# Performance work log

Hardware: AMD Instinct MI355X
Metric: run time of the kernel (lower is better)

Reference implementation:

```python
import jax, jax.numpy as jnp
import numpy as np

B, H, W, C, WS, SHIFT, NH = 64, 14, 14, 1024, 7, 3, 32
HD = C // NH
SCALE = HD ** -0.5

def _rel_index():
    coords = np.stack(np.meshgrid(np.arange(WS), np.arange(WS), indexing='ij'))  # [2,ws,ws]
    flat = coords.reshape(2, -1)
    rel = (flat[:, :, None] - flat[:, None, :]).transpose(1, 2, 0)  # [49,49,2]
    rel[:, :, 0] += WS - 1
    rel[:, :, 1] += WS - 1
    rel[:, :, 0] *= 2 * WS - 1
    return jnp.asarray(rel.sum(-1))  # [49,49] int

REL_IDX = _rel_index()

def _shift_mask():
    m = np.zeros((H, W), np.float32)
    cnt = 0
    for hs in (slice(0, -WS), slice(-WS, -SHIFT), slice(-SHIFT, None)):
        for ws_ in (slice(0, -WS), slice(-WS, -SHIFT), slice(-SHIFT, None)):
            m[hs, ws_] = cnt
            cnt += 1
    mw = m.reshape(H // WS, WS, W // WS, WS).transpose(0, 2, 1, 3).reshape(-1, WS * WS)
    diff = mw[:, None, :] - mw[:, :, None]
    return jnp.asarray(np.where(diff != 0, -100.0, 0.0).astype(np.float32))  # [nW,49,49]

ATTN_MASK = _shift_mask()

def layernorm(x, g, b, eps=1e-5):
    mu = x.mean(-1, keepdims=True)
    var = ((x - mu) ** 2).mean(-1, keepdims=True)
    return (x - mu) * jax.lax.rsqrt(var + eps) * g + b

def window_partition(x):  # [B,H,W,C] -> [B*nW, 49, C]
    x = x.reshape(B, H // WS, WS, W // WS, WS, C)
    return x.transpose(0, 1, 3, 2, 4, 5).reshape(-1, WS * WS, C)

def window_reverse(x):  # [B*nW, 49, C] -> [B,H,W,C]
    x = x.reshape(B, H // WS, W // WS, WS, WS, C)
    return x.transpose(0, 1, 3, 2, 4, 5).reshape(B, H, W, C)

def swin_block(x, p, shift):
    (ln1_g, ln1_b, qkv_w, qkv_b, rpb, proj_w, proj_b,
     ln2_g, ln2_b, fc1_w, fc1_b, fc2_w, fc2_b) = p
    h = layernorm(x, ln1_g, ln1_b).reshape(B, H, W, C)
    if shift:
        h = jnp.roll(h, (-SHIFT, -SHIFT), axis=(1, 2))
    hw = window_partition(h)                              # [Bn,49,C]
    qkv = hw @ qkv_w + qkv_b                              # [Bn,49,3C]
    q, k, v = qkv.reshape(-1, WS * WS, 3, NH, HD).transpose(2, 0, 3, 1, 4)  # each [Bn,NH,49,HD]
    attn = jnp.einsum('bhqd,bhkd->bhqk', q * SCALE, k)    # [Bn,NH,49,49]
    attn = attn + rpb[REL_IDX].transpose(2, 0, 1)[None]   # fused rel-pos bias
    if shift:
        nW = ATTN_MASK.shape[0]
        attn = attn.reshape(B, nW, NH, WS * WS, WS * WS) + ATTN_MASK[None, :, None]
        attn = attn.reshape(-1, NH, WS * WS, WS * WS)
    attn = jax.nn.softmax(attn, axis=-1)
    o = jnp.einsum('bhqk,bhkd->bhqd', attn, v).transpose(0, 2, 1, 3).reshape(-1, WS * WS, C)
    o = o @ proj_w + proj_b
    o = window_reverse(o)
    if shift:
        o = jnp.roll(o, (SHIFT, SHIFT), axis=(1, 2))
    x = x + o.reshape(B, H * W, C)
    h2 = layernorm(x, ln2_g, ln2_b)
    return x + jax.nn.gelu(h2 @ fc1_w + fc1_b, approximate=False) @ fc2_w + fc2_b

def setup_inputs() -> dict:
    key = jax.random.key(0)
    ks = iter(jax.random.split(key, 64))
    def rnd(shape, s=0.02):
        return jax.random.normal(next(ks), shape, jnp.float32) * s
    inp = {'x': jax.random.normal(next(ks), (B, H * W, C), jnp.float32)}
    for i in range(2):
        inp[f'b{i}_ln1_g'] = jnp.ones((C,), jnp.float32)
        inp[f'b{i}_ln1_b'] = jnp.zeros((C,), jnp.float32)
        inp[f'b{i}_qkv_w'] = rnd((C, 3 * C))
        inp[f'b{i}_qkv_b'] = jnp.zeros((3 * C,), jnp.float32)
        inp[f'b{i}_rpb'] = rnd(((2 * WS - 1) ** 2, NH))
        inp[f'b{i}_proj_w'] = rnd((C, C))
        inp[f'b{i}_proj_b'] = jnp.zeros((C,), jnp.float32)
        inp[f'b{i}_ln2_g'] = jnp.ones((C,), jnp.float32)
        inp[f'b{i}_ln2_b'] = jnp.zeros((C,), jnp.float32)
        inp[f'b{i}_fc1_w'] = rnd((C, 4 * C))
        inp[f'b{i}_fc1_b'] = jnp.zeros((4 * C,), jnp.float32)
        inp[f'b{i}_fc2_w'] = rnd((4 * C, C))
        inp[f'b{i}_fc2_b'] = jnp.zeros((C,), jnp.float32)
    inp['h_ln_g'] = jnp.ones((C,), jnp.float32)
    inp['h_ln_b'] = jnp.zeros((C,), jnp.float32)
    inp['h_w1'] = rnd((C, 512)); inp['h_b1'] = jnp.zeros((512,), jnp.float32)
    inp['h_w2'] = rnd((512, 128)); inp['h_b2'] = jnp.zeros((128,), jnp.float32)
    inp['h_w3'] = rnd((128, 2)); inp['h_b3'] = jnp.zeros((2,), jnp.float32)
    return inp

def reference(x,
              b0_ln1_g, b0_ln1_b, b0_qkv_w, b0_qkv_b, b0_rpb, b0_proj_w, b0_proj_b,
              b0_ln2_g, b0_ln2_b, b0_fc1_w, b0_fc1_b, b0_fc2_w, b0_fc2_b,
              b1_ln1_g, b1_ln1_b, b1_qkv_w, b1_qkv_b, b1_rpb, b1_proj_w, b1_proj_b,
              b1_ln2_g, b1_ln2_b, b1_fc1_w, b1_fc1_b, b1_fc2_w, b1_fc2_b,
              h_ln_g, h_ln_b, h_w1, h_b1, h_w2, h_b2, h_w3, h_b3):
    p0 = (b0_ln1_g, b0_ln1_b, b0_qkv_w, b0_qkv_b, b0_rpb, b0_proj_w, b0_proj_b,
          b0_ln2_g, b0_ln2_b, b0_fc1_w, b0_fc1_b, b0_fc2_w, b0_fc2_b)
    p1 = (b1_ln1_g, b1_ln1_b, b1_qkv_w, b1_qkv_b, b1_rpb, b1_proj_w, b1_proj_b,
          b1_ln2_g, b1_ln2_b, b1_fc1_w, b1_fc1_b, b1_fc2_w, b1_fc2_b)
    x = swin_block(x, p0, shift=False)
    x = swin_block(x, p1, shift=True)
    pooled = x.mean(axis=1)  # global avg pool -> [B, C]
    h = layernorm(pooled, h_ln_g, h_ln_b)
    h = jax.nn.gelu(h @ h_w1 + h_b1, approximate=False)  # dropout is identity (eval)
    h = jax.nn.gelu(h @ h_w2 + h_b2, approximate=False)
    return h @ h_w3 + h_b3  # [B, num_classes]
```

## Files before the change

### kernel.cpp

```cpp
#include <hip/hip_runtime.h>
#include <hip/hip_bf16.h>
#include <hip/hip_fp16.h>
#include <math.h>

#define BB 64
#define CC 1024
#define NH 32
#define NTOK (BB * 14 * 14)
#define SCALE 0.17677669529663687f

typedef __attribute__((ext_vector_type(8))) short short8;
typedef __attribute__((ext_vector_type(8))) unsigned short us8;
typedef __attribute__((ext_vector_type(4))) float f32x4;

__device__ __align__(16) float  g_X  [(size_t)NTOK * CC];
__device__ __align__(16) unsigned short g_Qh[(size_t)NTOK * 3072];
__device__ __align__(16) unsigned short g_B[(size_t)NTOK * CC];
__device__ __align__(16) unsigned short g_C[(size_t)NTOK * 4096];
__device__ __align__(16) unsigned short g_Wq[(size_t)2*3072*1024];
__device__ __align__(16) unsigned short g_Wp[(size_t)2*1024*1024];
__device__ __align__(16) unsigned short g_W1[(size_t)2*4096*1024];
__device__ __align__(16) unsigned short g_W2[(size_t)2*1024*4096];
__device__ __align__(16) float g_H0[64 * CC];
__device__ __align__(16) float g_H1[64 * 512];
__device__ __align__(16) float g_H2[64 * 128];

__device__ __forceinline__ float gelu_f(float x) {
    return 0.5f * x * (1.0f + erff(x * 0.70710678118654752f));
}

__device__ __forceinline__ unsigned short f16_bits(float v) {
    _Float16 hh = (_Float16)v;
    return *(unsigned short*)&hh;
}
__device__ __forceinline__ float f16_val(unsigned short u) {
    _Float16 h;
    __builtin_memcpy(&h, &u, 2);
    return (float)h;
}

__device__ __forceinline__ int win_to_xrow(int r, int shifted) {
    int bn = r / 49, t = r - bn * 49;
    int b = bn >> 2, w = bn & 3;
    int wh = w >> 1, ww_ = w & 1;
    int th = t / 7, tw = t - th * 7;
    int gh = wh * 7 + th, gw = ww_ * 7 + tw;
    if (shifted) { gh = gh + 3; if (gh >= 14) gh -= 14; gw = gw + 3; if (gw >= 14) gw -= 14; }
    return b * 196 + gh * 14 + gw;
}

__device__ __forceinline__ void gload_lds16(const void* g, void* l) {
    __builtin_amdgcn_global_load_lds(
        (const __attribute__((address_space(1))) unsigned int*)g,
        (__attribute__((address_space(3))) unsigned int*)l, 16, 0, 0);
}

__global__ __launch_bounds__(256) void convw_kernel(const float* __restrict__ W,
    unsigned short* __restrict__ Wh, int K, int N)
{
    __shared__ float t[32][33];
    int n0 = blockIdx.x * 32, k0 = blockIdx.y * 32;
    int tx = threadIdx.x & 31, ty = threadIdx.x >> 5;
    #pragma unroll
    for (int i = 0; i < 4; ++i)
        t[ty + 8 * i][tx] = W[(size_t)(k0 + ty + 8 * i) * N + n0 + tx];
    __syncthreads();
    #pragma unroll
    for (int i = 0; i < 4; ++i) {
        int n = ty + 8 * i;
        Wh[(size_t)(n0 + n) * K + k0 + tx] = f16_bits(t[tx][n]);
    }
}

__global__ __launch_bounds__(256) void ln_kernel(const float* __restrict__ X,
    const float* __restrict__ g, const float* __restrict__ bta,
    unsigned short* __restrict__ outh, int shifted, int partition)
{
    int token = blockIdx.x * 4 + (threadIdx.x >> 6);
    int lane = threadIdx.x & 63;
    int xrow = partition ? win_to_xrow(token, shifted) : token;
    const float4* src = (const float4*)(X + (size_t)xrow * CC);
    float4 v[4];
    float s = 0.f;
    #pragma unroll
    for (int w = 0; w < 4; ++w) {
        v[w] = src[w * 64 + lane];
        s += v[w].x + v[w].y + v[w].z + v[w].w;
    }
    #pragma unroll
    for (int o = 32; o; o >>= 1) s += __shfl_xor(s, o);
    float mean = s * (1.0f / CC);
    float ss = 0.f;
    #pragma unroll
    for (int w = 0; w < 4; ++w) {
        float d0 = v[w].x - mean, d1 = v[w].y - mean, d2 = v[w].z - mean, d3 = v[w].w - mean;
        ss += d0 * d0 + d1 * d1 + d2 * d2 + d3 * d3;
    }
    #pragma unroll
    for (int o = 32; o; o >>= 1) ss += __shfl_xor(ss, o);
    float inv = 1.0f / sqrtf(ss * (1.0f / CC) + 1e-5f);
    #pragma unroll
    for (int w = 0; w < 4; ++w) {
        int c4 = w * 64 + lane;
        float4 gv = *(const float4*)(g + c4 * 4);
        float4 bv = *(const float4*)(bta + c4 * 4);
        ushort4 uo;
        uo.x = f16_bits((v[w].x - mean) * inv * gv.x + bv.x);
        uo.y = f16_bits((v[w].y - mean) * inv * gv.y + bv.y);
        uo.z = f16_bits((v[w].z - mean) * inv * gv.z + bv.z);
        uo.w = f16_bits((v[w].w - mean) * inv * gv.w + bv.w);
        *(ushort4*)(outh + (size_t)token * CC + c4 * 4) = uo;
    }
}

template<int EPI>
__global__ __launch_bounds__(256, 2) void gemm_mfma(
    const unsigned short* __restrict__ A, const unsigned short* __restrict__ W,
    const float* __restrict__ bias,
    float* __restrict__ outf, unsigned short* __restrict__ outh,
    int N, int K, int shifted, int NR, int GC)
{
    __shared__ unsigned short sm[EPI <= 1 ? 16896 : 16640];
    const int tid = threadIdx.x;
    const int wave = tid >> 6, lane = tid & 63;
    const int wr = wave >> 1, wc = wave & 1;
    const int nb = gridDim.x;
    const int wg = (blockIdx.x & 7) * (nb >> 3) + (blockIdx.x >> 3);
    const int gsz = GC * NR;
    const int grp = wg / gsz;
    const int rem = wg - grp * gsz;
    const int by = rem / GC;
    const int bx = grp * GC + (rem - by * GC);
    const int row0 = by * 128, col0 = bx * 128;
    const int rsel = lane & 15;

    f32x4 acc[4][4] = {};

    const int srow = tid >> 3, sslot = tid & 7;

    for (int k0 = 0; k0 < K; k0 += 64) {
        #pragma unroll
        for (int i = 0; i < 8; ++i) {
            const int t = i >> 2;
            const int sub = i & 3;
            const int row = sub * 32 + srow;
            const int c = sslot ^ (row & 7);
            const unsigned short* gp = (t == 0) ? A : W;
            const int rb = (t == 0) ? row0 : col0;
            gload_lds16(gp + (size_t)(rb + row) * K + k0 + c * 8,
                        &sm[t * 8192 + sub * 2048 + tid * 8]);
        }
        __syncthreads();

        #pragma unroll
        for (int kk = 0; kk < 2; ++kk) {
            const int kc8 = kk * 4 + (lane >> 4);
            short8 fa[4], fw[4];
            #pragma unroll
            for (int m = 0; m < 4; ++m) {
                int ra = wr * 64 + m * 16 + rsel;
                fa[m] = *(const short8*)&sm[ra * 64 + ((kc8 ^ (ra & 7)) * 8)];
                int rw = wc * 64 + m * 16 + rsel;
                fw[m] = *(const short8*)&sm[8192 + rw * 64 + ((kc8 ^ (rw & 7)) * 8)];
            }
            #pragma unroll
            for (int m = 0; m < 4; ++m)
                #pragma unroll
                for (int n = 0; n < 4; ++n)
                    acc[m][n] = __builtin_amdgcn_mfma_f32_16x16x32_f16(fa[m], fw[n], acc[m][n], 0, 0, 0);
        }
        __syncthreads();
    }

    const int jrow = lane >> 4;
    if (EPI <= 1) {
        #pragma unroll
        for (int n = 0; n < 4; ++n) {
            int cl = wc * 64 + n * 16 + rsel;
            float bv = bias[col0 + cl];
            #pragma unroll
            for (int m = 0; m < 4; ++m)
                #pragma unroll
                for (int j = 0; j < 4; ++j) {
                    int rl = wr * 64 + m * 16 + jrow * 4 + j;
                    float v = acc[m][n][j] + bv;
                    if (EPI == 1) v = gelu_f(v);
                    sm[rl * 132 + cl] = f16_bits(v);
                }
        }
        __syncthreads();
        const int r = tid >> 1, cb = (tid & 1) * 64;
        unsigned short* dst = outh + (size_t)(row0 + r) * N + col0 + cb;
        const unsigned short* src = &sm[r * 132 + cb];
        #pragma unroll
        for (int i = 0; i < 8; ++i)
            *(us8*)(dst + i * 8) = *(const us8*)(src + i * 8);
    } else {
        float* smf = (float*)sm;
        const int rr = tid >> 2;
        const int cc4 = (tid & 3) * 32;
        #pragma unroll
        for (int half = 0; half < 2; ++half) {
            __syncthreads();
            if (wr == half) {
                #pragma unroll
                for (int n = 0; n < 4; ++n) {
                    const int cl = wc * 64 + n * 16 + rsel;
                    const float bv = bias[col0 + cl];
                    #pragma unroll
                    for (int m = 0; m < 4; ++m)
                        #pragma unroll
                        for (int j = 0; j < 4; ++j)
                            smf[(m * 16 + jrow * 4 + j) * 130 + cl] = acc[m][n][j] + bv;
                }
            }
            __syncthreads();
            const int gr = row0 + half * 64 + rr;
            const int orow = (EPI == 2) ? win_to_xrow(gr, shifted) : gr;
            float* dst = outf + (size_t)orow * CC + col0 + cc4;
            const float* srcl = &smf[rr * 130 + cc4];
            #pragma unroll
            for (int i = 0; i < 8; ++i) {
                float4 xv = *(float4*)(dst + i * 4);
                xv.x += srcl[i * 4 + 0];
                xv.y += srcl[i * 4 + 1];
                xv.z += srcl[i * 4 + 2];
                xv.w += srcl[i * 4 + 3];
                *(float4*)(dst + i * 4) = xv;
            }
        }
    }
}

__global__ __launch_bounds__(256) void attn_kernel(const unsigned short* __restrict__ qkv,
    unsigned short* __restrict__ oh, const float* __restrict__ rpb, int shifted)
{
    int blk = blockIdx.x;
    int bn = blk >> 3;
    int hg = blk & 7;
    int wv = threadIdx.x >> 6;
    int lane = threadIdx.x & 63;
    int h = hg * 4 + wv;

    __shared__ float ks[4][49][32], vs[4][49][32];

    for (int idx = lane; idx < 49 * 32; idx += 64) {
        int t = idx >> 5, d = idx & 31;
        const unsigned short* p = qkv + (size_t)(bn * 49 + t) * 3072 + h * 32 + d;
        ks[wv][t][d] = f16_val(p[1024]);
        vs[wv][t][d] = f16_val(p[2048]);
    }
    __syncthreads();

    if (lane < 49) {
        const int i = lane;
        const int ih = i / 7, iw = i - ih * 7;
        const int w = bn & 3, wh = w >> 1, ww_ = w & 1;
        const int gh = wh * 7 + ih, gw = ww_ * 7 + iw;
        const int li = (gh < 7 ? 0 : (gh < 11 ? 1 : 2)) * 3 + (gw < 7 ? 0 : (gw < 11 ? 1 : 2));

        float qreg[32];
        const unsigned short* qp = qkv + (size_t)(bn * 49 + i) * 3072 + h * 32;
        #pragma unroll
        for (int d8 = 0; d8 < 4; ++d8) {
            us8 qv = *(const us8*)(qp + d8 * 8);
            #pragma unroll
            for (int e = 0; e < 8; ++e) {
                unsigned short u = qv[e];
                qreg[d8 * 8 + e] = f16_val(u) * SCALE;
            }
        }

        float p[49];
        float mx = -1e30f;
        #pragma unroll
        for (int j = 0; j < 49; ++j) {
            const int jh = j / 7, jw = j - jh * 7;
            float dot = 0.f;
            #pragma unroll
            for (int d = 0; d < 32; ++d) dot = fmaf(qreg[d], ks[wv][j][d], dot);
            const int ridx = (ih - jh + 6) * 13 + (iw - jw + 6);
            float val = dot + rpb[ridx * 32 + h];
            if (shifted) {
                const int gjh = wh * 7 + jh, gjw = ww_ * 7 + jw;
                const int lj = (gjh < 7 ? 0 : (gjh < 11 ? 1 : 2)) * 3 +
                               (gjw < 7 ? 0 : (gjw < 11 ? 1 : 2));
                if (li != lj) val -= 100.0f;
            }
            p[j] = val;
            mx = fmaxf(mx, val);
        }
        float denom = 0.f;
        #pragma unroll
        for (int j = 0; j < 49; ++j) {
            p[j] = expf(p[j] - mx);
            denom += p[j];
        }
        const float rd = 1.0f / denom;

        unsigned short* orow = oh + (size_t)(bn * 49 + i) * CC + h * 32;
        #pragma unroll 4
        for (int d = 0; d < 32; ++d) {
            float acc = 0.f;
            #pragma unroll
            for (int j = 0; j < 49; ++j) acc = fmaf(p[j], vs[wv][j][d], acc);
            orow[d] = f16_bits(acc * rd);
        }
    }
}

__global__ __launch_bounds__(256) void pool_ln_kernel(const float* __restrict__ X,
    const float* __restrict__ g, const float* __restrict__ bta, float* __restrict__ out)
{
    int b = blockIdx.x, tid = threadIdx.x;
    int lane = tid & 63, wid = tid >> 6;
    const float* base = X + (size_t)b * 196 * CC + tid * 4;
    float a0 = 0, a1 = 0, a2 = 0, a3 = 0;
    for (int t = 0; t < 196; ++t) {
        float4 v = *(const float4*)(base + (size_t)t * CC);
        a0 += v.x; a1 += v.y; a2 += v.z; a3 += v.w;
    }
    const float inv196 = 1.0f / 196.0f;
    float p0 = a0 * inv196, p1 = a1 * inv196, p2 = a2 * inv196, p3 = a3 * inv196;
    float s = p0 + p1 + p2 + p3;
    #pragma unroll
    for (int o = 32; o; o >>= 1) s += __shfl_xor(s, o);
    __shared__ float sred[4], ssred[4];
    if (lane == 0) sred[wid] = s;
    __syncthreads();
    float mean = (sred[0] + sred[1] + sred[2] + sred[3]) * (1.0f / CC);
    float d0 = p0 - mean, d1 = p1 - mean, d2 = p2 - mean, d3 = p3 - mean;
    float ss = d0 * d0 + d1 * d1 + d2 * d2 + d3 * d3;
    #pragma unroll
    for (int o = 32; o; o >>= 1) ss += __shfl_xor(ss, o);
    if (lane == 0) ssred[wid] = ss;
    __syncthreads();
    float var = (ssred[0] + ssred[1] + ssred[2] + ssred[3]) * (1.0f / CC);
    float inv = 1.0f / sqrtf(var + 1e-5f);
    float4 gv = *(const float4*)(g + tid * 4);
    float4 bv = *(const float4*)(bta + tid * 4);
    float4 o4;
    o4.x = d0 * inv * gv.x + bv.x;
    o4.y = d1 * inv * gv.y + bv.y;
    o4.z = d2 * inv * gv.z + bv.z;
    o4.w = d3 * inv * gv.w + bv.w;
    *(float4*)(out + (size_t)b * CC + tid * 4) = o4;
}

__global__ __launch_bounds__(256) void head_rowgemm(const float* __restrict__ A,
    const float* __restrict__ W, const float* __restrict__ bias,
    float* __restrict__ out, int K, int N, int act)
{
    __shared__ float As[1024];
    int r = blockIdx.x, tid = threadIdx.x;
    for (int k = tid; k < K; k += 256) As[k] = A[(size_t)r * K + k];
    __syncthreads();
    for (int c = tid; c < N; c += 256) {
        float s0 = 0.f, s1 = 0.f;
        for (int k = 0; k < K; k += 2) {
            s0 = fmaf(As[k],     W[(size_t)k * N + c],       s0);
            s1 = fmaf(As[k + 1], W[(size_t)(k + 1) * N + c], s1);
        }
        float s = s0 + s1 + bias[c];
        out[(size_t)r * N + c] = act ? gelu_f(s) : s;
    }
}

extern "C" void kernel_launch(void* const* d_in, const int* in_sizes, int n_in,
                              void* d_out, int out_size, void* d_ws, size_t ws_size,
                              hipStream_t stream) {
    const float* x = (const float*)d_in[0];
    auto P = [&](int i) { return (const float*)d_in[i]; };

    float *X, *H0, *H1, *H2;
    unsigned short *QKVh, *B, *C, *Wq, *Wp, *W1, *W2;
    { void* p;
      hipGetSymbolAddress(&p, HIP_SYMBOL(g_X));   X    = (float*)p;
      hipGetSymbolAddress(&p, HIP_SYMBOL(g_Qh));  QKVh = (unsigned short*)p;
      hipGetSymbolAddress(&p, HIP_SYMBOL(g_B));   B    = (unsigned short*)p;
      hipGetSymbolAddress(&p, HIP_SYMBOL(g_C));   C    = (unsigned short*)p;
      hipGetSymbolAddress(&p, HIP_SYMBOL(g_Wq));  Wq   = (unsigned short*)p;
      hipGetSymbolAddress(&p, HIP_SYMBOL(g_Wp));  Wp   = (unsigned short*)p;
      hipGetSymbolAddress(&p, HIP_SYMBOL(g_W1));  W1   = (unsigned short*)p;
      hipGetSymbolAddress(&p, HIP_SYMBOL(g_W2));  W2   = (unsigned short*)p;
      hipGetSymbolAddress(&p, HIP_SYMBOL(g_H0));  H0 = (float*)p;
      hipGetSymbolAddress(&p, HIP_SYMBOL(g_H1));  H1 = (float*)p;
      hipGetSymbolAddress(&p, HIP_SYMBOL(g_H2));  H2 = (float*)p;
    }

    hipMemcpyAsync(X, x, (size_t)NTOK * CC * sizeof(float),
                   hipMemcpyDeviceToDevice, stream);

    for (int blk = 0; blk < 2; ++blk) {
        int base = 1 + blk * 13;
        convw_kernel<<<dim3(3072/32, 1024/32), 256, 0, stream>>>(
            P(base + 2), Wq + (size_t)blk*3072*1024, 1024, 3072);
        convw_kernel<<<dim3(1024/32, 1024/32), 256, 0, stream>>>(
            P(base + 5), Wp + (size_t)blk*1024*1024, 1024, 1024);
        convw_kernel<<<dim3(4096/32, 1024/32), 256, 0, stream>>>(
            P(base + 9), W1 + (size_t)blk*4096*1024, 1024, 4096);
        convw_kernel<<<dim3(1024/32, 4096/32), 256, 0, stream>>>(
            P(base + 11), W2 + (size_t)blk*1024*4096, 4096, 1024);
    }

    for (int blk = 0; blk < 2; ++blk) {
        int base = 1 + blk * 13;
        const float *ln1g = P(base + 0), *ln1b = P(base + 1);
        const float *qkvb = P(base + 3);
        const float *rpb  = P(base + 4);
        const float *projb = P(base + 6);
        const float *ln2g = P(base + 7), *ln2b = P(base + 8);
        const float *fc1b = P(base + 10);
        const float *fc2b = P(base + 12);
        int shifted = blk;
        const unsigned short* wq = Wq + (size_t)blk*3072*1024;
        const unsigned short* wp = Wp + (size_t)blk*1024*1024;
        const unsigned short* w1 = W1 + (size_t)blk*4096*1024;
        const unsigned short* w2 = W2 + (size_t)blk*1024*4096;

        ln_kernel<<<NTOK / 4, 256, 0, stream>>>(X, ln1g, ln1b, B, shifted, 1);
        gemm_mfma<0><<<2352, 256, 0, stream>>>(
            B, wq, qkvb, nullptr, QKVh, 3072, 1024, 0, 98, 8);
        attn_kernel<<<256 * 8, 256, 0, stream>>>(QKVh, B, rpb, shifted);
        gemm_mfma<2><<<784, 256, 0, stream>>>(
            B, wp, projb, X, nullptr, 1024, 1024, shifted, 98, 8);
        ln_kernel<<<NTOK / 4, 256, 0, stream>>>(X, ln2g, ln2b, B, 0, 0);
        gemm_mfma<1><<<3136, 256, 0, stream>>>(
            B, w1, fc1b, nullptr, C, 4096, 1024, 0, 98, 8);
        gemm_mfma<3><<<784, 256, 0, stream>>>(
            C, w2, fc2b, X, nullptr, 1024, 4096, 0, 98, 8);
    }

    pool_ln_kernel<<<64, 256, 0, stream>>>(X, P(27), P(28), H0);
    head_rowgemm<<<64, 256, 0, stream>>>(H0, P(29), P(30), H1, 1024, 512, 1);
    head_rowgemm<<<64, 256, 0, stream>>>(H1, P(31), P(32), H2, 512, 128, 1);
    head_rowgemm<<<64, 256, 0, stream>>>(H2, P(33), P(34), (float*)d_out, 128, 2, 0);
}
```

Baseline: 1.542 ms.

## Enlarge GEMM tile to 256x128 with 512-thread blocks

Doubles the GEMM block tile along M from 128 to 256 rows and uses 8 waves (512 threads) per block. The weight tile is now shared by twice as many A rows, which cuts global traffic for the weight operand. Epilogues are restructured to stage output in halves or quarters through LDS, and the grid sizes shrink to match. The trade-off is fewer blocks in flight (392 for the 1024-column GEMMs) and larger LDS use, which may lower occupancy and worsen tail effects on a many-CU device.

```diff
diff --git a/kernel.cpp b/kernel.cpp
--- a/kernel.cpp
+++ b/kernel.cpp
@@ -114,13 +114,13 @@
 }
 
 template<int EPI>
-__global__ __launch_bounds__(256, 2) void gemm_mfma(
+__global__ __launch_bounds__(512) void gemm_mfma(
     const unsigned short* __restrict__ A, const unsigned short* __restrict__ W,
     const float* __restrict__ bias,
     float* __restrict__ outf, unsigned short* __restrict__ outh,
     int N, int K, int shifted, int NR, int GC)
 {
-    __shared__ unsigned short sm[EPI <= 1 ? 16896 : 16640];
+    __shared__ unsigned short sm[24576];
     const int tid = threadIdx.x;
     const int wave = tid >> 6, lane = tid & 63;
     const int wr = wave >> 1, wc = wave & 1;
@@ -131,7 +131,7 @@
     const int rem = wg - grp * gsz;
     const int by = rem / GC;
     const int bx = grp * GC + (rem - by * GC);
-    const int row0 = by * 128, col0 = bx * 128;
+    const int row0 = by * 256, col0 = bx * 128;
     const int rsel = lane & 15;
 
     f32x4 acc[4][4] = {};
@@ -140,15 +140,18 @@
 
     for (int k0 = 0; k0 < K; k0 += 64) {
         #pragma unroll
-        for (int i = 0; i < 8; ++i) {
-            const int t = i >> 2;
-            const int sub = i & 3;
-            const int row = sub * 32 + srow;
+        for (int sub = 0; sub < 4; ++sub) {
+            const int row = sub * 64 + srow;
             const int c = sslot ^ (row & 7);
-            const unsigned short* gp = (t == 0) ? A : W;
-            const int rb = (t == 0) ? row0 : col0;
-            gload_lds16(gp + (size_t)(rb + row) * K + k0 + c * 8,
-                        &sm[t * 8192 + sub * 2048 + tid * 8]);
+            gload_lds16(A + (size_t)(row0 + row) * K + k0 + c * 8,
+                        &sm[sub * 4096 + tid * 8]);
+        }
+        #pragma unroll
+        for (int sub = 0; sub < 2; ++sub) {
+            const int row = sub * 64 + srow;
+            const int c = sslot ^ (row & 7);
+            gload_lds16(W + (size_t)(col0 + row) * K + k0 + c * 8,
+                        &sm[16384 + sub * 4096 + tid * 8]);
         }
         __syncthreads();
 
@@ -161,7 +164,7 @@
                 int ra = wr * 64 + m * 16 + rsel;
                 fa[m] = *(const short8*)&sm[ra * 64 + ((kc8 ^ (ra & 7)) * 8)];
                 int rw = wc * 64 + m * 16 + rsel;
-                fw[m] = *(const short8*)&sm[8192 + rw * 64 + ((kc8 ^ (rw & 7)) * 8)];
+                fw[m] = *(const short8*)&sm[16384 + rw * 64 + ((kc8 ^ (rw & 7)) * 8)];
             }
             #pragma unroll
             for (int m = 0; m < 4; ++m)
@@ -175,34 +178,40 @@
     const int jrow = lane >> 4;
     if (EPI <= 1) {
         #pragma unroll
-        for (int n = 0; n < 4; ++n) {
-            int cl = wc * 64 + n * 16 + rsel;
-            float bv = bias[col0 + cl];
-            #pragma unroll
-            for (int m = 0; m < 4; ++m)
+        for (int half = 0; half < 2; ++half) {
+            __syncthreads();
+            if ((wr >> 1) == half) {
                 #pragma unroll
-                for (int j = 0; j < 4; ++j) {
-                    int rl = wr * 64 + m * 16 + jrow * 4 + j;
-                    float v = acc[m][n][j] + bv;
-                    if (EPI == 1) v = gelu_f(v);
-                    sm[rl * 132 + cl] = f16_bits(v);
+                for (int n = 0; n < 4; ++n) {
+                    int cl = wc * 64 + n * 16 + rsel;
+                    float bv = bias[col0 + cl];
+                    #pragma unroll
+                    for (int m = 0; m < 4; ++m)
+                        #pragma unroll
+                        for (int j = 0; j < 4; ++j) {
+                            int rl = (wr & 1) * 64 + m * 16 + jrow * 4 + j;
+                            float v = acc[m][n][j] + bv;
+                            if (EPI == 1) v = gelu_f(v);
+                            sm[rl * 132 + cl] = f16_bits(v);
+                        }
                 }
-        }
-        __syncthreads();
-        const int r = tid >> 1, cb = (tid & 1) * 64;
-        unsigned short* dst = outh + (size_t)(row0 + r) * N + col0 + cb;
-        const unsigned short* src = &sm[r * 132 + cb];
-        #pragma unroll
-        for (int i = 0; i < 8; ++i)
-            *(us8*)(dst + i * 8) = *(const us8*)(src + i * 8);
+            }
+            __syncthreads();
+            const int r = tid >> 2, cb = (tid & 3) * 32;
+            unsigned short* dst = outh + (size_t)(row0 + half * 128 + r) * N + col0 + cb;
+            const unsigned short* src = &sm[r * 132 + cb];
+            #pragma unroll
+            for (int i = 0; i < 4; ++i)
+                *(us8*)(dst + i * 8) = *(const us8*)(src + i * 8);
+        }
     } else {
         float* smf = (float*)sm;
-        const int rr = tid >> 2;
-        const int cc4 = (tid & 3) * 32;
-        #pragma unroll
-        for (int half = 0; half < 2; ++half) {
+        const int rr = tid >> 3;
+        const int cc4 = (tid & 7) * 16;
+        #pragma unroll
+        for (int q = 0; q < 4; ++q) {
             __syncthreads();
-            if (wr == half) {
+            if (wr == q) {
                 #pragma unroll
                 for (int n = 0; n < 4; ++n) {
                     const int cl = wc * 64 + n * 16 + rsel;
@@ -215,12 +224,12 @@
                 }
             }
             __syncthreads();
-            const int gr = row0 + half * 64 + rr;
+            const int gr = row0 + q * 64 + rr;
             const int orow = (EPI == 2) ? win_to_xrow(gr, shifted) : gr;
             float* dst = outf + (size_t)orow * CC + col0 + cc4;
             const float* srcl = &smf[rr * 130 + cc4];
             #pragma unroll
-            for (int i = 0; i < 8; ++i) {
+            for (int i = 0; i < 4; ++i) {
                 float4 xv = *(float4*)(dst + i * 4);
                 xv.x += srcl[i * 4 + 0];
                 xv.y += srcl[i * 4 + 1];
@@ -419,16 +428,16 @@
         const unsigned short* w2 = W2 + (size_t)blk*1024*4096;
 
         ln_kernel<<<NTOK / 4, 256, 0, stream>>>(X, ln1g, ln1b, B, shifted, 1);
-        gemm_mfma<0><<<2352, 256, 0, stream>>>(
-            B, wq, qkvb, nullptr, QKVh, 3072, 1024, 0, 98, 8);
+        gemm_mfma<0><<<1176, 512, 0, stream>>>(
+            B, wq, qkvb, nullptr, QKVh, 3072, 1024, 0, 49, 8);
         attn_kernel<<<256 * 8, 256, 0, stream>>>(QKVh, B, rpb, shifted);
-        gemm_mfma<2><<<784, 256, 0, stream>>>(
-            B, wp, projb, X, nullptr, 1024, 1024, shifted, 98, 8);
+        gemm_mfma<2><<<392, 512, 0, stream>>>(
+            B, wp, projb, X, nullptr, 1024, 1024, shifted, 49, 8);
         ln_kernel<<<NTOK / 4, 256, 0, stream>>>(X, ln2g, ln2b, B, 0, 0);
-        gemm_mfma<1><<<3136, 256, 0, stream>>>(
-            B, w1, fc1b, nullptr, C, 4096, 1024, 0, 98, 8);
-        gemm_mfma<3><<<784, 256, 0, stream>>>(
-            C, w2, fc2b, X, nullptr, 1024, 4096, 0, 98, 8);
+        gemm_mfma<1><<<1568, 512, 0, stream>>>(
+            B, w1, fc1b, nullptr, C, 4096, 1024, 0, 49, 8);
+        gemm_mfma<3><<<392, 512, 0, stream>>>(
+            C, w2, fc2b, X, nullptr, 1024, 4096, 0, 49, 8);
     }
 
     pool_ln_kernel<<<64, 256, 0, stream>>>(X, P(27), P(28), H0);
```

Result: no change. 1.565 ms (+1.5%).
